# Kernel optimization log

Hardware: AMD Instinct MI355X
Metric: run time of the kernel (lower is better)

Reference implementation:

```python
import jax, jax.numpy as jnp
import numpy as np

B, T, E = 2, 2048, 1024
H, Dh = 16, 64  # num_heads, head_size; H*Dh == E


def setup_inputs() -> dict:
    key = jax.random.key(0)
    ks = jax.random.split(key, 5)
    s = 0.02
    return {
        "x": jax.random.normal(ks[0], (B, T, E), dtype=jnp.float32),
        "Wq": jax.random.normal(ks[1], (E, H * Dh), dtype=jnp.float32) * s,
        "Wk": jax.random.normal(ks[2], (E, H * Dh), dtype=jnp.float32) * s,
        "Wv": jax.random.normal(ks[3], (E, H * Dh), dtype=jnp.float32) * s,
        "Wo": jax.random.normal(ks[4], (H * Dh, E), dtype=jnp.float32) * s,
        "bo": jnp.zeros((E,), dtype=jnp.float32),
    }


def reference(x, Wq, Wk, Wv, Wo, bo):
    # Batched equivalent of the per-head Python loop: each head's bias-free
    # q/k/v Linear is one column-block of Wq/Wk/Wv.
    b, t, e = x.shape
    q = (x @ Wq).reshape(b, t, H, Dh)  # [B,T,H,Dh]
    k = (x @ Wk).reshape(b, t, H, Dh)
    v = (x @ Wv).reshape(b, t, H, Dh)

    scale = 1.0 / jnp.sqrt(jnp.asarray(Dh, dtype=x.dtype))
    scores = jnp.einsum("bqhd,bkhd->bhqk", q, k) * scale  # [B,H,T,T]
    causal = jnp.tril(jnp.ones((t, t), dtype=bool))
    scores = jnp.where(causal[None, None, :, :], scores, jnp.asarray(-jnp.inf, dtype=x.dtype))
    attn = jax.nn.softmax(scores, axis=-1)

    out = jnp.einsum("bhqk,bkhd->bqhd", attn, v).reshape(b, t, H * Dh)  # concat heads
    return out @ Wo + bo  # output projection (dropout is identity at p=0)
```

## Files before the change

### kernel.cpp

```cpp
#include <hip/hip_runtime.h>
#include <hip/hip_bf16.h>

typedef __attribute__((ext_vector_type(8))) short bf16x8;
typedef __attribute__((ext_vector_type(4))) float f32x4;
typedef __attribute__((ext_vector_type(4))) unsigned short u16x4;

__device__ __forceinline__ unsigned short f2bf(float f) {
    union { float f; unsigned int i; } x; x.f = f;
    unsigned int lsb = (x.i >> 16) & 1u;
    x.i += 0x7fffu + lsb;
    return (unsigned short)(x.i >> 16);
}

__device__ __forceinline__ void gl_lds16(const unsigned short* g, unsigned short* l) {
    __builtin_amdgcn_global_load_lds(
        (const __attribute__((address_space(1))) void*)g,
        (__attribute__((address_space(3))) void*)l, 16, 0, 0);
}

__device__ __forceinline__ unsigned int cvt_pk_bf16(float lo, float hi) {
    unsigned int d;
    asm("v_cvt_pk_bf16_f32 %0, %1, %2" : "=v"(d) : "v"(lo), "v"(hi));
    return d;
}

__device__ __forceinline__ bf16x8 pf_build_s(f32x4 pa, f32x4 pb, float s) {
    unsigned int E0 = cvt_pk_bf16(pa[0] * s, pa[1] * s);
    unsigned int O0 = cvt_pk_bf16(pa[2] * s, pa[3] * s);
    unsigned int E1 = cvt_pk_bf16(pb[0] * s, pb[1] * s);
    unsigned int O1 = cvt_pk_bf16(pb[2] * s, pb[3] * s);
    asm("v_permlane32_swap_b32 %0, %1" : "+v"(E0), "+v"(E1));
    asm("v_permlane32_swap_b32 %0, %1" : "+v"(O0), "+v"(O1));
    asm("v_permlane16_swap_b32 %0, %1" : "+v"(E0), "+v"(E1));
    asm("v_permlane16_swap_b32 %0, %1" : "+v"(O0), "+v"(O1));
    union { unsigned int u[4]; bf16x8 v; } r;
    r.u[0] = E0; r.u[1] = O0; r.u[2] = E1; r.u[3] = O1;
    return r.v;
}

__global__ __launch_bounds__(256) void prep(
    const float* __restrict__ x,
    const float* __restrict__ Wq, const float* __restrict__ Wk,
    const float* __restrict__ Wv, const float* __restrict__ Wo,
    unsigned short* __restrict__ xb,
    unsigned short* __restrict__ WqkvT, unsigned short* __restrict__ WoT)
{
    const int E = 1024;
    const int bid = blockIdx.x;
    __shared__ float t[32][33];

    if (bid < 4096) {
        int i = bid * 256 + threadIdx.x;
        f32x4 v = ((const f32x4*)x)[i];
        u16x4 o;
#pragma unroll
        for (int j = 0; j < 4; ++j) o[j] = f2bf(v[j]);
        ((u16x4*)xb)[i] = o;
        return;
    }
    const int r = bid - 4096;
    const int which = r >> 10;
    const int sub = r & 1023;
    const float* src = which == 0 ? Wq : which == 1 ? Wk : which == 2 ? Wv : Wo;
    unsigned short* dst = which == 3 ? WoT : WqkvT + (size_t)which * E * E;

    const int tx = threadIdx.x & 31, ty = threadIdx.x >> 5;
    const int n0 = (sub & 31) * 32, k0 = (sub >> 5) * 32;
#pragma unroll
    for (int i = 0; i < 4; ++i)
        t[ty + 8 * i][tx] = src[(size_t)(k0 + ty + 8 * i) * E + n0 + tx];
    __syncthreads();
#pragma unroll
    for (int i = 0; i < 4; ++i)
        dst[(size_t)(n0 + ty + 8 * i) * E + k0 + tx] = f2bf(t[tx][ty + 8 * i]);
}

template <int PERM>
__global__ __launch_bounds__(256) void gemm128(
    const unsigned short* __restrict__ A,
    const unsigned short* __restrict__ BT,
    const float* __restrict__ bias,
    float* __restrict__ Cf,
    unsigned short* __restrict__ q_out,
    unsigned short* __restrict__ k_out,
    unsigned short* __restrict__ v_out,
    int M, int N, int K)
{
    __shared__ __align__(16) unsigned short As[128 * 32];
    __shared__ __align__(16) unsigned short Bs[128 * 32];

    const int tid  = threadIdx.x;
    const int wave = tid >> 6;
    const int lane = tid & 63;
    const int ln15 = lane & 15;
    const int kg   = lane >> 4;
    const int bm = blockIdx.x * 128, bn = blockIdx.y * 128;
    const int wm = (wave >> 1) * 64, wn = (wave & 1) * 64;

    const bool swap = (PERM == 0) || (bn < 2048);

    f32x4 acc[4][4];
#pragma unroll
    for (int i = 0; i < 4; ++i)
#pragma unroll
        for (int j = 0; j < 4; ++j) acc[i][j] = (f32x4){0.f, 0.f, 0.f, 0.f};

    const int sr = wave * 32 + (lane >> 2);
    const int sc = (lane & 3) * 8;

    for (int k0 = 0; k0 < K; k0 += 32) {
        gl_lds16(A  + (size_t)(bm + sr)      * K + k0 + sc, As + wave * 1024);
        gl_lds16(A  + (size_t)(bm + sr + 16) * K + k0 + sc, As + wave * 1024 + 512);
        gl_lds16(BT + (size_t)(bn + sr)      * K + k0 + sc, Bs + wave * 1024);
        gl_lds16(BT + (size_t)(bn + sr + 16) * K + k0 + sc, Bs + wave * 1024 + 512);
        __syncthreads();

        bf16x8 af[4], bw[4];
#pragma unroll
        for (int mt = 0; mt < 4; ++mt)
            af[mt] = *(const bf16x8*)&As[(wm + mt * 16 + ln15) * 32 + kg * 8];
#pragma unroll
        for (int nt = 0; nt < 4; ++nt)
            bw[nt] = *(const bf16x8*)&Bs[(wn + nt * 16 + ln15) * 32 + kg * 8];
        if (swap) {
#pragma unroll
            for (int mt = 0; mt < 4; ++mt)
#pragma unroll
                for (int nt = 0; nt < 4; ++nt)
                    acc[mt][nt] = __builtin_amdgcn_mfma_f32_16x16x32_bf16(
                        bw[nt], af[mt], acc[mt][nt], 0, 0, 0);
        } else {
#pragma unroll
            for (int mt = 0; mt < 4; ++mt)
#pragma unroll
                for (int nt = 0; nt < 4; ++nt)
                    acc[mt][nt] = __builtin_amdgcn_mfma_f32_16x16x32_bf16(
                        af[mt], bw[nt], acc[mt][nt], 0, 0, 0);
        }
        __syncthreads();
    }

    if (PERM == 0) {
#pragma unroll
        for (int mt = 0; mt < 4; ++mt) {
            const int row = bm + wm + mt * 16 + ln15;
#pragma unroll
            for (int nt = 0; nt < 4; ++nt) {
                const int c0 = bn + wn + nt * 16 + kg * 4;
                f32x4 bv = *(const f32x4*)(bias + c0);
                f32x4 o;
#pragma unroll
                for (int r = 0; r < 4; ++r) o[r] = acc[mt][nt][r] + bv[r];
                *(f32x4*)(Cf + (size_t)row * N + c0) = o;
            }
        }
    } else {
        const int sec = bn >> 10;
        if (sec < 2) {
            unsigned short* dst = sec == 0 ? q_out : k_out;
            const float scale = sec == 0 ? 0.125f : 1.0f;
#pragma unroll
            for (int mt = 0; mt < 4; ++mt) {
                const int tg = bm + wm + mt * 16 + ln15;
                const int b = tg >> 11, t = tg & 2047;
#pragma unroll
                for (int np = 0; np < 2; ++np) {
                    const int c0 = bn + wn + np * 32 + kg * 8;
                    const int h = (c0 >> 6) & 15, d0 = c0 & 63;
                    bf16x8 pf = pf_build_s(acc[mt][2 * np], acc[mt][2 * np + 1], scale);
                    *(bf16x8*)(dst + ((size_t)(b * 16 + h) * 2048 + t) * 64 + d0) = pf;
                }
            }
        } else {
#pragma unroll
            for (int nt = 0; nt < 4; ++nt) {
                const int c = bn + wn + nt * 16 + ln15;
                const int h = (c >> 6) & 15, d = c & 63;
#pragma unroll
                for (int mp = 0; mp < 2; ++mp) {
                    const int t0 = bm + wm + mp * 32 + kg * 8;
                    const int b = t0 >> 11, t = t0 & 2047;
                    bf16x8 pf = pf_build_s(acc[2 * mp][nt], acc[2 * mp + 1][nt], 1.0f);
                    *(bf16x8*)(v_out + ((size_t)(b * 16 + h) * 64 + d) * 2048 + t) = pf;
                }
            }
        }
    }
}

__device__ __forceinline__ void softmax_tile(
    f32x4 sr[4], bool diag, int q_loc, int kg,
    bf16x8& pf0, bf16x8& pf1, f32x4& accl, bf16x8 ones)
{
    if (diag) {
#pragma unroll
        for (int kt = 0; kt < 4; ++kt)
#pragma unroll
            for (int r = 0; r < 4; ++r)
                if (kt * 16 + kg * 4 + r > q_loc) sr[kt][r] = -1e30f;
    }
    f32x4 pe[4];
#pragma unroll
    for (int kt = 0; kt < 4; ++kt)
#pragma unroll
        for (int r = 0; r < 4; ++r) pe[kt][r] = __expf(sr[kt][r]);
    pf0 = pf_build_s(pe[0], pe[1], 1.0f);
    pf1 = pf_build_s(pe[2], pe[3], 1.0f);
    accl = __builtin_amdgcn_mfma_f32_16x16x32_bf16(pf0, ones, accl, 0, 0, 0);
    accl = __builtin_amdgcn_mfma_f32_16x16x32_bf16(pf1, ones, accl, 0, 0, 0);
}

__global__ __launch_bounds__(256) void flash_attn(
    const unsigned short* __restrict__ Q,
    const unsigned short* __restrict__ Km,
    const unsigned short* __restrict__ Vtg,
    unsigned short* __restrict__ O,
    int T, int H)
{
    __shared__ __align__(16) unsigned short Ks[2][64][72];
    __shared__ __align__(16) unsigned short Vs[2][64][72];

    const int tid  = threadIdx.x;
    const int wave = tid >> 6;
    const int lane = tid & 63;
    const int ln15 = lane & 15;
    const int kg   = lane >> 4;
    const int sA   = blockIdx.x;
    const int sB   = (T >> 6) - 1 - sA;
    const int kmax = sB;
    const int bh   = blockIdx.y;
    const int b    = bh >> 4, h = bh & 15;
    const size_t base  = (size_t)bh * T * 64;
    const size_t vbase = (size_t)bh * 64 * T;
    const int q_loc = wave * 16 + ln15;

    bf16x8 qf[2][2];
    {
        const unsigned short* QrA = Q + base + (size_t)(sA * 64 + q_loc) * 64;
        const unsigned short* QrB = Q + base + (size_t)(sB * 64 + q_loc) * 64;
        qf[0][0] = *(const bf16x8*)(QrA + kg * 8);
        qf[0][1] = *(const bf16x8*)(QrA + 32 + kg * 8);
        qf[1][0] = *(const bf16x8*)(QrB + kg * 8);
        qf[1][1] = *(const bf16x8*)(QrB + 32 + kg * 8);
    }

    bf16x8 ones;
    {
        const short o = (ln15 == 0) ? (short)0x3F80 : (short)0;
#pragma unroll
        for (int j = 0; j < 8; ++j) ones[j] = o;
    }

    f32x4 o_acc[2][4];
#pragma unroll
    for (int s = 0; s < 2; ++s)
#pragma unroll
        for (int dt = 0; dt < 4; ++dt) o_acc[s][dt] = (f32x4){0.f, 0.f, 0.f, 0.f};
    f32x4 acc_l[2] = {(f32x4){0.f, 0.f, 0.f, 0.f}, (f32x4){0.f, 0.f, 0.f, 0.f}};

    const int sky = tid >> 3;
    const int sd  = (tid & 7) * 8;

    bf16x8 pk0, pk1, pv0, pv1;
    pk0 = *(const bf16x8*)(Km + base + (size_t)sky * 64 + sd);
    pk1 = *(const bf16x8*)(Km + base + (size_t)(sky + 32) * 64 + sd);
    pv0 = *(const bf16x8*)(Vtg + vbase + (size_t)sky * T + sd);
    pv1 = *(const bf16x8*)(Vtg + vbase + (size_t)(sky + 32) * T + sd);

    for (int kb = 0; kb <= kmax; ++kb) {
        const int bufi = kb & 1;
        *(bf16x8*)&Ks[bufi][sky][sd]      = pk0;
        *(bf16x8*)&Ks[bufi][sky + 32][sd] = pk1;
        *(bf16x8*)&Vs[bufi][sky][sd]      = pv0;
        *(bf16x8*)&Vs[bufi][sky + 32][sd] = pv1;
        if (kb < kmax) {
            const int kn = (kb + 1) * 64;
            pk0 = *(const bf16x8*)(Km + base + (size_t)(kn + sky) * 64 + sd);
            pk1 = *(const bf16x8*)(Km + base + (size_t)(kn + sky + 32) * 64 + sd);
            pv0 = *(const bf16x8*)(Vtg + vbase + (size_t)sky * T + kn + sd);
            pv1 = *(const bf16x8*)(Vtg + vbase + (size_t)(sky + 32) * T + kn + sd);
        }
        __syncthreads();

        const bool doA = (kb <= sA);

        f32x4 srB[4], srA[4];
#pragma unroll
        for (int kt = 0; kt < 4; ++kt) {
            bf16x8 kf0 = *(const bf16x8*)&Ks[bufi][kt * 16 + ln15][kg * 8];
            bf16x8 kf1 = *(const bf16x8*)&Ks[bufi][kt * 16 + ln15][32 + kg * 8];
            f32x4 a = (f32x4){0.f, 0.f, 0.f, 0.f};
            a = __builtin_amdgcn_mfma_f32_16x16x32_bf16(kf0, qf[1][0], a, 0, 0, 0);
            a = __builtin_amdgcn_mfma_f32_16x16x32_bf16(kf1, qf[1][1], a, 0, 0, 0);
            srB[kt] = a;
            if (doA) {
                f32x4 c = (f32x4){0.f, 0.f, 0.f, 0.f};
                c = __builtin_amdgcn_mfma_f32_16x16x32_bf16(kf0, qf[0][0], c, 0, 0, 0);
                c = __builtin_amdgcn_mfma_f32_16x16x32_bf16(kf1, qf[0][1], c, 0, 0, 0);
                srA[kt] = c;
            }
        }

        bf16x8 pfB0, pfB1, pfA0, pfA1;
        softmax_tile(srB, kb == sB, q_loc, kg, pfB0, pfB1, acc_l[1], ones);
        if (doA)
            softmax_tile(srA, kb == sA, q_loc, kg, pfA0, pfA1, acc_l[0], ones);

#pragma unroll
        for (int dt = 0; dt < 4; ++dt) {
            bf16x8 vf0 = *(const bf16x8*)&Vs[bufi][dt * 16 + ln15][kg * 8];
            bf16x8 vf1 = *(const bf16x8*)&Vs[bufi][dt * 16 + ln15][32 + kg * 8];
            o_acc[1][dt] = __builtin_amdgcn_mfma_f32_16x16x32_bf16(pfB0, vf0, o_acc[1][dt], 0, 0, 0);
            o_acc[1][dt] = __builtin_amdgcn_mfma_f32_16x16x32_bf16(pfB1, vf1, o_acc[1][dt], 0, 0, 0);
            if (doA) {
                o_acc[0][dt] = __builtin_amdgcn_mfma_f32_16x16x32_bf16(pfA0, vf0, o_acc[0][dt], 0, 0, 0);
                o_acc[0][dt] = __builtin_amdgcn_mfma_f32_16x16x32_bf16(pfA1, vf1, o_acc[0][dt], 0, 0, 0);
            }
        }
    }

#pragma unroll
    for (int s = 0; s < 2; ++s) {
        const int qb = (s == 0 ? sA : sB) * 64;
        float inv[4];
#pragma unroll
        for (int r = 0; r < 4; ++r)
            inv[r] = 1.0f / __shfl(acc_l[s][r], lane & 48, 64);
#pragma unroll
        for (int dt = 0; dt < 4; ++dt)
#pragma unroll
            for (int r = 0; r < 4; ++r) {
                const int t = qb + wave * 16 + kg * 4 + r;
                const int d = dt * 16 + ln15;
                O[(size_t)(b * T + t) * (H * 64) + h * 64 + d] =
                    f2bf(o_acc[s][dt][r] * inv[r]);
            }
    }
}

extern "C" void kernel_launch(void* const* d_in, const int* in_sizes, int n_in,
                              void* d_out, int out_size, void* d_ws, size_t ws_size,
                              hipStream_t stream)
{
    const int B = 2, T = 2048, E = 1024, H = 16;
    const int M = B * T;

    const float* x  = (const float*)d_in[0];
    const float* Wq = (const float*)d_in[1];
    const float* Wk = (const float*)d_in[2];
    const float* Wv = (const float*)d_in[3];
    const float* Wo = (const float*)d_in[4];
    const float* bo = (const float*)d_in[5];
    float* out = (float*)d_out;

    unsigned short* xb     = (unsigned short*)d_ws;
    unsigned short* WqkvT  = xb + (size_t)M * E;
    unsigned short* WoT    = WqkvT + (size_t)3 * E * E;
    unsigned short* q      = WoT + (size_t)E * E;
    unsigned short* k      = q + (size_t)M * E;
    unsigned short* vT     = k + (size_t)M * E;
    unsigned short* ao     = vT + (size_t)M * E;

    prep<<<8192, 256, 0, stream>>>(x, Wq, Wk, Wv, Wo, xb, WqkvT, WoT);

    dim3 g1(M / 128, 3 * E / 128);
    gemm128<1><<<g1, 256, 0, stream>>>(xb, WqkvT, nullptr, nullptr, q, k, vT,
                                       M, 3 * E, E);

    dim3 ag(T / 128, B * H);
    flash_attn<<<ag, 256, 0, stream>>>(q, k, vT, ao, T, H);

    dim3 g2(M / 128, E / 128);
    gemm128<0><<<g2, 256, 0, stream>>>(ao, WoT, bo, out, nullptr, nullptr, nullptr,
                                       M, E, E);
}
```

Measured before the change: 208.7 us.

## Shrink GEMM tiles to 64x64, split QKV launch, remap attention blocks per XCD

The GEMM kernel moves from 128x128 to 64x64 tiles, and the fused QKV projection becomes two launches, one for Q/K and one for V with its transposed store. The attention kernel remaps block indices so each of the 8 XCDs handles four whole (b,h) heads, and it raises wave priority around the MFMA sections with s_setprio. Smaller tiles give more blocks to fill the CUs, but each block reuses less data from LDS and global memory, and the extra launch adds its own overhead.

New measurement: 188.8 us. -9.5%, faster.

```diff
diff --git a/kernel.cpp b/kernel.cpp
--- a/kernel.cpp
+++ b/kernel.cpp
@@ -75,8 +75,8 @@
         dst[(size_t)(n0 + ty + 8 * i) * E + k0 + tx] = f2bf(t[tx][ty + 8 * i]);
 }
 
-template <int PERM>
-__global__ __launch_bounds__(256) void gemm128(
+template <int MODE>
+__global__ __launch_bounds__(256) void gemm64(
     const unsigned short* __restrict__ A,
     const unsigned short* __restrict__ BT,
     const float* __restrict__ bias,
@@ -86,66 +86,62 @@
     unsigned short* __restrict__ v_out,
     int M, int N, int K)
 {
-    __shared__ __align__(16) unsigned short As[128 * 32];
-    __shared__ __align__(16) unsigned short Bs[128 * 32];
+    __shared__ __align__(16) unsigned short As[64 * 32];
+    __shared__ __align__(16) unsigned short Bs[64 * 32];
 
     const int tid  = threadIdx.x;
     const int wave = tid >> 6;
     const int lane = tid & 63;
     const int ln15 = lane & 15;
     const int kg   = lane >> 4;
-    const int bm = blockIdx.x * 128, bn = blockIdx.y * 128;
-    const int wm = (wave >> 1) * 64, wn = (wave & 1) * 64;
-
-    const bool swap = (PERM == 0) || (bn < 2048);
-
-    f32x4 acc[4][4];
-#pragma unroll
-    for (int i = 0; i < 4; ++i)
-#pragma unroll
-        for (int j = 0; j < 4; ++j) acc[i][j] = (f32x4){0.f, 0.f, 0.f, 0.f};
-
-    const int sr = wave * 32 + (lane >> 2);
-    const int sc = (lane & 3) * 8;
+    const int bm = blockIdx.x * 64, bn = blockIdx.y * 64;
+    const int wm = (wave >> 1) * 32, wn = (wave & 1) * 32;
+
+    f32x4 acc[2][2];
+#pragma unroll
+    for (int i = 0; i < 2; ++i)
+#pragma unroll
+        for (int j = 0; j < 2; ++j) acc[i][j] = (f32x4){0.f, 0.f, 0.f, 0.f};
+
+    const int sr  = wave * 16 + (lane >> 2);
+    const int scl = (lane & 3) * 8;
 
     for (int k0 = 0; k0 < K; k0 += 32) {
-        gl_lds16(A  + (size_t)(bm + sr)      * K + k0 + sc, As + wave * 1024);
-        gl_lds16(A  + (size_t)(bm + sr + 16) * K + k0 + sc, As + wave * 1024 + 512);
-        gl_lds16(BT + (size_t)(bn + sr)      * K + k0 + sc, Bs + wave * 1024);
-        gl_lds16(BT + (size_t)(bn + sr + 16) * K + k0 + sc, Bs + wave * 1024 + 512);
+        gl_lds16(A  + (size_t)(bm + sr) * K + k0 + scl, As + wave * 512);
+        gl_lds16(BT + (size_t)(bn + sr) * K + k0 + scl, Bs + wave * 512);
         __syncthreads();
 
-        bf16x8 af[4], bw[4];
-#pragma unroll
-        for (int mt = 0; mt < 4; ++mt)
+        bf16x8 af[2], bw[2];
+#pragma unroll
+        for (int mt = 0; mt < 2; ++mt)
             af[mt] = *(const bf16x8*)&As[(wm + mt * 16 + ln15) * 32 + kg * 8];
 #pragma unroll
-        for (int nt = 0; nt < 4; ++nt)
+        for (int nt = 0; nt < 2; ++nt)
             bw[nt] = *(const bf16x8*)&Bs[(wn + nt * 16 + ln15) * 32 + kg * 8];
-        if (swap) {
-#pragma unroll
-            for (int mt = 0; mt < 4; ++mt)
-#pragma unroll
-                for (int nt = 0; nt < 4; ++nt)
+        if (MODE == 2) {
+#pragma unroll
+            for (int mt = 0; mt < 2; ++mt)
+#pragma unroll
+                for (int nt = 0; nt < 2; ++nt)
+                    acc[mt][nt] = __builtin_amdgcn_mfma_f32_16x16x32_bf16(
+                        af[mt], bw[nt], acc[mt][nt], 0, 0, 0);
+        } else {
+#pragma unroll
+            for (int mt = 0; mt < 2; ++mt)
+#pragma unroll
+                for (int nt = 0; nt < 2; ++nt)
                     acc[mt][nt] = __builtin_amdgcn_mfma_f32_16x16x32_bf16(
                         bw[nt], af[mt], acc[mt][nt], 0, 0, 0);
-        } else {
-#pragma unroll
-            for (int mt = 0; mt < 4; ++mt)
-#pragma unroll
-                for (int nt = 0; nt < 4; ++nt)
-                    acc[mt][nt] = __builtin_amdgcn_mfma_f32_16x16x32_bf16(
-                        af[mt], bw[nt], acc[mt][nt], 0, 0, 0);
         }
         __syncthreads();
     }
 
-    if (PERM == 0) {
-#pragma unroll
-        for (int mt = 0; mt < 4; ++mt) {
+    if (MODE == 0) {
+#pragma unroll
+        for (int mt = 0; mt < 2; ++mt) {
             const int row = bm + wm + mt * 16 + ln15;
 #pragma unroll
-            for (int nt = 0; nt < 4; ++nt) {
+            for (int nt = 0; nt < 2; ++nt) {
                 const int c0 = bn + wn + nt * 16 + kg * 4;
                 f32x4 bv = *(const f32x4*)(bias + c0);
                 f32x4 o;
@@ -154,36 +150,28 @@
                 *(f32x4*)(Cf + (size_t)row * N + c0) = o;
             }
         }
+    } else if (MODE == 1) {
+        const int sec = bn >> 10;
+        unsigned short* dst = sec == 0 ? q_out : k_out;
+        const float scale = sec == 0 ? 0.125f : 1.0f;
+        const int c0 = bn + wn + kg * 8;
+        const int h = (c0 >> 6) & 15, d0 = c0 & 63;
+#pragma unroll
+        for (int mt = 0; mt < 2; ++mt) {
+            const int tg = bm + wm + mt * 16 + ln15;
+            const int b = tg >> 11, t = tg & 2047;
+            bf16x8 pf = pf_build_s(acc[mt][0], acc[mt][1], scale);
+            *(bf16x8*)(dst + ((size_t)(b * 16 + h) * 2048 + t) * 64 + d0) = pf;
+        }
     } else {
-        const int sec = bn >> 10;
-        if (sec < 2) {
-            unsigned short* dst = sec == 0 ? q_out : k_out;
-            const float scale = sec == 0 ? 0.125f : 1.0f;
-#pragma unroll
-            for (int mt = 0; mt < 4; ++mt) {
-                const int tg = bm + wm + mt * 16 + ln15;
-                const int b = tg >> 11, t = tg & 2047;
-#pragma unroll
-                for (int np = 0; np < 2; ++np) {
-                    const int c0 = bn + wn + np * 32 + kg * 8;
-                    const int h = (c0 >> 6) & 15, d0 = c0 & 63;
-                    bf16x8 pf = pf_build_s(acc[mt][2 * np], acc[mt][2 * np + 1], scale);
-                    *(bf16x8*)(dst + ((size_t)(b * 16 + h) * 2048 + t) * 64 + d0) = pf;
-                }
-            }
-        } else {
-#pragma unroll
-            for (int nt = 0; nt < 4; ++nt) {
-                const int c = bn + wn + nt * 16 + ln15;
-                const int h = (c >> 6) & 15, d = c & 63;
-#pragma unroll
-                for (int mp = 0; mp < 2; ++mp) {
-                    const int t0 = bm + wm + mp * 32 + kg * 8;
-                    const int b = t0 >> 11, t = t0 & 2047;
-                    bf16x8 pf = pf_build_s(acc[2 * mp][nt], acc[2 * mp + 1][nt], 1.0f);
-                    *(bf16x8*)(v_out + ((size_t)(b * 16 + h) * 64 + d) * 2048 + t) = pf;
-                }
-            }
+        const int t0 = bm + wm + kg * 8;
+        const int b = t0 >> 11, t = t0 & 2047;
+#pragma unroll
+        for (int nt = 0; nt < 2; ++nt) {
+            const int c = bn + wn + nt * 16 + ln15;
+            const int h = c >> 6, d = c & 63;
+            bf16x8 pf = pf_build_s(acc[0][nt], acc[1][nt], 1.0f);
+            *(bf16x8*)(v_out + ((size_t)(b * 16 + h) * 64 + d) * 2048 + t) = pf;
         }
     }
 }
@@ -225,10 +213,15 @@
     const int lane = tid & 63;
     const int ln15 = lane & 15;
     const int kg   = lane >> 4;
-    const int sA   = blockIdx.x;
+
+    const int flat = blockIdx.y * gridDim.x + blockIdx.x;
+    const int xcd  = flat & 7;
+    const int slot = flat >> 3;
+    const int bh   = xcd * 4 + (slot >> 4);
+    const int sA   = slot & 15;
+
     const int sB   = (T >> 6) - 1 - sA;
     const int kmax = sB;
-    const int bh   = blockIdx.y;
     const int b    = bh >> 4, h = bh & 15;
     const size_t base  = (size_t)bh * T * 64;
     const size_t vbase = (size_t)bh * 64 * T;
@@ -285,6 +278,7 @@
         const bool doA = (kb <= sA);
 
         f32x4 srB[4], srA[4];
+        __builtin_amdgcn_s_setprio(1);
 #pragma unroll
         for (int kt = 0; kt < 4; ++kt) {
             bf16x8 kf0 = *(const bf16x8*)&Ks[bufi][kt * 16 + ln15][kg * 8];
@@ -300,12 +294,14 @@
                 srA[kt] = c;
             }
         }
+        __builtin_amdgcn_s_setprio(0);
 
         bf16x8 pfB0, pfB1, pfA0, pfA1;
         softmax_tile(srB, kb == sB, q_loc, kg, pfB0, pfB1, acc_l[1], ones);
         if (doA)
             softmax_tile(srA, kb == sA, q_loc, kg, pfA0, pfA1, acc_l[0], ones);
 
+        __builtin_amdgcn_s_setprio(1);
 #pragma unroll
         for (int dt = 0; dt < 4; ++dt) {
             bf16x8 vf0 = *(const bf16x8*)&Vs[bufi][dt * 16 + ln15][kg * 8];
@@ -317,6 +313,7 @@
                 o_acc[0][dt] = __builtin_amdgcn_mfma_f32_16x16x32_bf16(pfA1, vf1, o_acc[0][dt], 0, 0, 0);
             }
         }
+        __builtin_amdgcn_s_setprio(0);
     }
 
 #pragma unroll
@@ -363,14 +360,17 @@
 
     prep<<<8192, 256, 0, stream>>>(x, Wq, Wk, Wv, Wo, xb, WqkvT, WoT);
 
-    dim3 g1(M / 128, 3 * E / 128);
-    gemm128<1><<<g1, 256, 0, stream>>>(xb, WqkvT, nullptr, nullptr, q, k, vT,
-                                       M, 3 * E, E);
+    dim3 gqk(M / 64, 2 * E / 64);
+    gemm64<1><<<gqk, 256, 0, stream>>>(xb, WqkvT, nullptr, nullptr,
+                                       q, k, nullptr, M, 2 * E, E);
+    dim3 gv(M / 64, E / 64);
+    gemm64<2><<<gv, 256, 0, stream>>>(xb, WqkvT + (size_t)2 * E * E, nullptr,
+                                      nullptr, nullptr, nullptr, vT, M, E, E);
 
     dim3 ag(T / 128, B * H);
     flash_attn<<<ag, 256, 0, stream>>>(q, k, vT, ao, T, H);
 
-    dim3 g2(M / 128, E / 128);
-    gemm128<0><<<g2, 256, 0, stream>>>(ao, WoT, bo, out, nullptr, nullptr, nullptr,
-                                       M, E, E);
-}
+    dim3 g2(M / 64, E / 64);
+    gemm64<0><<<g2, 256, 0, stream>>>(ao, WoT, bo, out, nullptr, nullptr,
+                                      nullptr, M, E, E);
+}
```
